# Kernel tuning notes

Hardware: AMD Instinct MI355X
Metric: run time of the kernel (lower is better)

The kernel has to match this reference:

```python
import jax, jax.numpy as jnp
import numpy as np

B, S, D = 8, 2048, 768
N_SPANS = 512
MAX_W = 30  # static max span width (inclusive width in tokens)
H = 100
NEG = -1e30


def setup_inputs() -> dict:
    key = jax.random.key(0)
    k1, k2, k3, k4, k5, k6 = jax.random.split(key, 6)
    seq_tensor = jax.random.normal(k1, (B, S, D), dtype=jnp.float32)
    starts = jax.random.randint(k2, (B, N_SPANS), 0, S - MAX_W)
    widths = jax.random.randint(k3, (B, N_SPANS), 1, MAX_W + 1)  # span length in [1, MAX_W]
    ends_excl = starts + widths  # exclusive end, as module expects
    span_indices = jnp.stack([starts, ends_excl], axis=-1).astype(jnp.int64)
    span_mask = (jax.random.uniform(k4, (B, N_SPANS)) > 0.1).astype(jnp.int32)
    att_w = jax.random.normal(k5, (D, 1), dtype=jnp.float32) / np.sqrt(D)
    att_b = jnp.zeros((1,), dtype=jnp.float32)
    ffnn_w = jax.random.normal(k6, (D, H), dtype=jnp.float32) / np.sqrt(D)
    ffnn_b = jnp.zeros((H,), dtype=jnp.float32)
    return {"seq_tensor": seq_tensor, "span_indices": span_indices, "span_mask": span_mask,
            "att_w": att_w, "att_b": att_b, "ffnn_w": ffnn_w, "ffnn_b": ffnn_b}


def reference(seq_tensor, span_indices, span_mask, att_w, att_b, ffnn_w, ffnn_b):
    # exclusive end -> inclusive end (span_end_is_exclusive=True)
    starts = span_indices[..., 0]
    ends = span_indices[..., 1] - 1
    widths = ends - starts  # inclusive width - 1, in [0, MAX_W-1]

    offsets = jnp.arange(MAX_W)  # [W]
    raw_idx = starts[..., None] + offsets  # [B, N, W]
    width_mask = offsets <= widths[..., None]  # [B, N, W]
    idx = jnp.where(width_mask, raw_idx, 0)

    # global attention logits over the sequence: [B, S]
    att_logits = (jnp.einsum('bsd,do->bso', seq_tensor, att_w) + att_b)[..., 0]

    # gather span token embeddings and logits: [B, N, W, D], [B, N, W]
    span_emb = jax.vmap(lambda seq, i: seq[i])(seq_tensor, idx)
    span_logits = jax.vmap(lambda lg, i: lg[i])(att_logits, idx)

    # masked softmax over span width
    span_logits = jnp.where(width_mask, span_logits, NEG)
    attn = jax.nn.softmax(span_logits, axis=-1)  # [B, N, W]

    attended = jnp.einsum('bnw,bnwd->bnd', attn, span_emb)  # [B, N, D]
    attended = attended * span_mask.astype(attended.dtype)[..., None]

    # FeedForward: 1 layer Linear + tanh (dropout=0)
    out = jnp.tanh(jnp.einsum('bnd,dh->bnh', attended, ffnn_w) + ffnn_b)
    return out
```

## Files before the change

kernel.cpp:

```cpp
#include <hip/hip_runtime.h>
#include <cstdint>
#include <cstddef>

#define NB 8
#define NS 2048
#define ND 768
#define NSP 512
#define MAXW 30
#define NH 100
#define LDP 104
#define NKS 24
#define NCF 8
#define BM 16
#define NIT 12

typedef __attribute__((ext_vector_type(8))) _Float16 half8;
typedef __attribute__((ext_vector_type(2))) __fp16 fp16x2;
typedef __attribute__((ext_vector_type(4))) float floatx4;

union U4H8 { uint4 v; half8 h8; unsigned u[4]; unsigned short us[8]; };
union H2U  { fp16x2 h; unsigned u; };

__device__ inline unsigned short f2h(float f) {
    _Float16 h = (_Float16)f;
    union { _Float16 hh; unsigned short us; } c; c.hh = h;
    return c.us;
}

__global__ __launch_bounds__(64) void pack_b_kernel(
    const float* __restrict__ ffnn_w, const float* __restrict__ att_w,
    uint4* __restrict__ Bfrag)
{
    const int ks = blockIdx.x >> 3, cf = blockIdx.x & 7;
    const int lane = threadIdx.x;
    const int q = lane >> 4, r = lane & 15;
    const int n = cf * 16 + r;
    U4H8 p;
#pragma unroll
    for (int j = 0; j < 8; j++) {
        int k = ks * 32 + q * 8 + j;
        float v = (n < NH) ? ffnn_w[(size_t)k * NH + n]
                           : (n == NH ? att_w[k] : 0.f);
        p.us[j] = f2h(v);
    }
    Bfrag[(size_t)(ks * NCF + cf) * 64 + lane] = p.v;
}

__global__ __launch_bounds__(256, 4) void proj_kernel(
    const float* __restrict__ seq, const uint4* __restrict__ Bfrag,
    float* __restrict__ P, float* __restrict__ Lg)
{
    __shared__ unsigned Ah[2][BM][36];
    const int t = threadIdx.x;
    const int wave = t >> 6, lane = t & 63;
    const int q = lane >> 4, r = lane & 15;
    const int cf0 = wave * 2;
    const int row0 = blockIdx.x * BM;

    floatx4 acc[2] = {{0.f,0.f,0.f,0.f},{0.f,0.f,0.f,0.f}};

    const int sr = t >> 4, sc = t & 15;
    const floatx4* gA = (const floatx4*)(seq + (size_t)(row0 + sr) * ND);
    floatx4 sv = __builtin_nontemporal_load(gA + sc);

    const uint4* bp = Bfrag + (size_t)cf0 * 64 + lane;
    uint4 Bc0 = bp[0], Bc1 = bp[64], Bc2 = bp[512], Bc3 = bp[512 + 64];

    for (int i = 0; i < NIT; ++i) {
        H2U u01, u23;
        u01.h = __builtin_amdgcn_cvt_pkrtz(sv.x, sv.y);
        u23.h = __builtin_amdgcn_cvt_pkrtz(sv.z, sv.w);
        { uint2 u; u.x = u01.u; u.y = u23.u; *(uint2*)&Ah[i & 1][sr][sc * 2] = u; }
        __syncthreads();

        const int ni = (i + 1 < NIT) ? i + 1 : i;
        sv = __builtin_nontemporal_load(gA + ni * 16 + sc);
        const size_t nb = (size_t)ni * 1024;
        uint4 Bn0 = bp[nb], Bn1 = bp[nb + 64], Bn2 = bp[nb + 512], Bn3 = bp[nb + 512 + 64];

#pragma unroll
        for (int ksl = 0; ksl < 2; ++ksl) {
            U4H8 a, b0, b1;
            a.v  = *(const uint4*)&Ah[i & 1][r][ksl * 16 + q * 4];
            b0.v = ksl ? Bc2 : Bc0;
            b1.v = ksl ? Bc3 : Bc1;
            acc[0] = __builtin_amdgcn_mfma_f32_16x16x32_f16(a.h8, b0.h8, acc[0], 0, 0, 0);
            acc[1] = __builtin_amdgcn_mfma_f32_16x16x32_f16(a.h8, b1.h8, acc[1], 0, 0, 0);
        }
        Bc0 = Bn0; Bc1 = Bn1; Bc2 = Bn2; Bc3 = Bn3;
    }

#pragma unroll
    for (int c = 0; c < 2; ++c) {
        const int col = (cf0 + c) * 16 + r;
        const int rowb = row0 + q * 4;
        if (col < NH) {
#pragma unroll
            for (int reg = 0; reg < 4; ++reg)
                P[(size_t)(rowb + reg) * LDP + col] = acc[c][reg];
        } else if (col == NH) {
#pragma unroll
            for (int reg = 0; reg < 4; ++reg)
                Lg[rowb + reg] = acc[c][reg];
        }
    }
}

__global__ __launch_bounds__(256, 4) void span_kernel(
    const int* __restrict__ span_idx, const int* __restrict__ span_mask,
    const float* __restrict__ P, const float* __restrict__ Lg,
    const float* __restrict__ ffnn_b, float* __restrict__ out)
{
    const int hw = threadIdx.x >> 5, lane = threadIdx.x & 31;
    const int gs = blockIdx.x * 8 + hw;
    const int b = gs / NSP;
    const int st = span_idx[2 * gs];
    int w = span_idx[2 * gs + 1] - st;
    w = max(1, min(w, MAXW));

    float lg = (lane < w) ? Lg[b * NS + st + lane] : -1e30f;
    float mx = lg;
#pragma unroll
    for (int off = 16; off > 0; off >>= 1) mx = fmaxf(mx, __shfl_xor(mx, off, 32));
    float e = (lane < w) ? __expf(lg - mx) : 0.f;
    float sum = e;
#pragma unroll
    for (int off = 16; off > 0; off >>= 1) sum += __shfl_xor(sum, off, 32);
    float attn = e / sum;

    int cl = min(lane, 24);
    const float4* Pb4 = (const float4*)(P + ((size_t)b * NS + st) * LDP) + cl;
    float4 acc = {0.f, 0.f, 0.f, 0.f};
#pragma unroll
    for (int i = 0; i < MAXW; ++i) {
        float a = __shfl(attn, i, 32);
        if (i < w) {
            float4 v = Pb4[i * (LDP / 4)];
            acc.x += a * v.x; acc.y += a * v.y; acc.z += a * v.z; acc.w += a * v.w;
        }
    }

    if (lane < 25) {
        float m = (float)span_mask[gs];
        float4 bias = ((const float4*)ffnn_b)[lane];
        float4 o;
        o.x = tanhf(m * acc.x + bias.x);
        o.y = tanhf(m * acc.y + bias.y);
        o.z = tanhf(m * acc.z + bias.z);
        o.w = tanhf(m * acc.w + bias.w);
        *(float4*)(out + (size_t)gs * NH + 4 * lane) = o;
    }
}

extern "C" void kernel_launch(void* const* d_in, const int* in_sizes, int n_in,
                              void* d_out, int out_size, void* d_ws, size_t ws_size,
                              hipStream_t stream) {
    const float* seq      = (const float*)d_in[0];
    const int*   span_idx = (const int*)d_in[1];
    const int*   span_msk = (const int*)d_in[2];
    const float* att_w    = (const float*)d_in[3];
    const float* ffnn_w   = (const float*)d_in[5];
    const float* ffnn_b   = (const float*)d_in[6];
    float* out = (float*)d_out;

    char* ws = (char*)d_ws;
    size_t off = 0;
    float* P     = (float*)(ws + off); off += (size_t)NB * NS * LDP * 4;
    uint4* Bfrag = (uint4*)(ws + off); off += (size_t)NKS * NCF * 64 * 16;
    float* Lg    = (float*)(ws + off);

    pack_b_kernel<<<NKS * NCF, 64, 0, stream>>>(ffnn_w, att_w, Bfrag);
    proj_kernel<<<(NB * NS) / BM, 256, 0, stream>>>(seq, Bfrag, P, Lg);
    span_kernel<<<(NB * NSP) / 8, 256, 0, stream>>>(span_idx, span_msk, P, Lg, ffnn_b, out);
}
```

Measured before the change: 122.4 us.

## Double projection row tile to 32 rows per block to reuse B fragments

Each proj_kernel block now covers 32 sequence rows instead of 16. Every wave reuses its loaded weight fragments across two 16-row MFMA tiles, which halves B-fragment global traffic per row and halves the block count. The A-tile staging changes so each thread loads two float4 per k-step, and the nontemporal loads become regular loads. The cost is more registers and accumulators per thread, which may lower occupancy, and fewer blocks to hide latency in what is likely a bandwidth-bound read of the sequence.

New measurement: 113.8 us. -7.0%, faster.

```diff
diff --git a/kernel.cpp b/kernel.cpp
--- a/kernel.cpp
+++ b/kernel.cpp
@@ -11,7 +11,7 @@
 #define LDP 104
 #define NKS 24
 #define NCF 8
-#define BM 16
+#define BM 32
 #define NIT 12
 
 typedef __attribute__((ext_vector_type(8))) _Float16 half8;
@@ -57,51 +57,63 @@
     const int cf0 = wave * 2;
     const int row0 = blockIdx.x * BM;
 
-    floatx4 acc[2] = {{0.f,0.f,0.f,0.f},{0.f,0.f,0.f,0.f}};
+    floatx4 acc[2][2] = {{{0.f,0.f,0.f,0.f},{0.f,0.f,0.f,0.f}},
+                         {{0.f,0.f,0.f,0.f},{0.f,0.f,0.f,0.f}}};
 
-    const int sr = t >> 4, sc = t & 15;
-    const floatx4* gA = (const floatx4*)(seq + (size_t)(row0 + sr) * ND);
-    floatx4 sv = __builtin_nontemporal_load(gA + sc);
+    const int sr = t >> 3, sc = t & 7;
+    const float4* gA = (const float4*)(seq + (size_t)(row0 + sr) * ND);
+    float4 sv0 = gA[sc], sv1 = gA[sc + 8];
 
     const uint4* bp = Bfrag + (size_t)cf0 * 64 + lane;
     uint4 Bc0 = bp[0], Bc1 = bp[64], Bc2 = bp[512], Bc3 = bp[512 + 64];
 
     for (int i = 0; i < NIT; ++i) {
-        H2U u01, u23;
-        u01.h = __builtin_amdgcn_cvt_pkrtz(sv.x, sv.y);
-        u23.h = __builtin_amdgcn_cvt_pkrtz(sv.z, sv.w);
-        { uint2 u; u.x = u01.u; u.y = u23.u; *(uint2*)&Ah[i & 1][sr][sc * 2] = u; }
+        H2U a01, a23, b01, b23;
+        a01.h = __builtin_amdgcn_cvt_pkrtz(sv0.x, sv0.y);
+        a23.h = __builtin_amdgcn_cvt_pkrtz(sv0.z, sv0.w);
+        b01.h = __builtin_amdgcn_cvt_pkrtz(sv1.x, sv1.y);
+        b23.h = __builtin_amdgcn_cvt_pkrtz(sv1.z, sv1.w);
+        { uint2 u; u.x = a01.u; u.y = a23.u; *(uint2*)&Ah[i & 1][sr][sc * 2] = u; }
+        { uint2 u; u.x = b01.u; u.y = b23.u; *(uint2*)&Ah[i & 1][sr][sc * 2 + 16] = u; }
         __syncthreads();
 
         const int ni = (i + 1 < NIT) ? i + 1 : i;
-        sv = __builtin_nontemporal_load(gA + ni * 16 + sc);
+        sv0 = gA[ni * 16 + sc];
+        sv1 = gA[ni * 16 + sc + 8];
         const size_t nb = (size_t)ni * 1024;
         uint4 Bn0 = bp[nb], Bn1 = bp[nb + 64], Bn2 = bp[nb + 512], Bn3 = bp[nb + 512 + 64];
 
 #pragma unroll
         for (int ksl = 0; ksl < 2; ++ksl) {
-            U4H8 a, b0, b1;
-            a.v  = *(const uint4*)&Ah[i & 1][r][ksl * 16 + q * 4];
+            U4H8 b0, b1;
             b0.v = ksl ? Bc2 : Bc0;
             b1.v = ksl ? Bc3 : Bc1;
-            acc[0] = __builtin_amdgcn_mfma_f32_16x16x32_f16(a.h8, b0.h8, acc[0], 0, 0, 0);
-            acc[1] = __builtin_amdgcn_mfma_f32_16x16x32_f16(a.h8, b1.h8, acc[1], 0, 0, 0);
+#pragma unroll
+            for (int rt = 0; rt < 2; ++rt) {
+                U4H8 a;
+                a.v = *(const uint4*)&Ah[i & 1][rt * 16 + r][ksl * 16 + q * 4];
+                acc[rt][0] = __builtin_amdgcn_mfma_f32_16x16x32_f16(a.h8, b0.h8, acc[rt][0], 0, 0, 0);
+                acc[rt][1] = __builtin_amdgcn_mfma_f32_16x16x32_f16(a.h8, b1.h8, acc[rt][1], 0, 0, 0);
+            }
         }
         Bc0 = Bn0; Bc1 = Bn1; Bc2 = Bn2; Bc3 = Bn3;
     }
 
 #pragma unroll
-    for (int c = 0; c < 2; ++c) {
-        const int col = (cf0 + c) * 16 + r;
-        const int rowb = row0 + q * 4;
-        if (col < NH) {
+    for (int rt = 0; rt < 2; ++rt) {
 #pragma unroll
-            for (int reg = 0; reg < 4; ++reg)
-                P[(size_t)(rowb + reg) * LDP + col] = acc[c][reg];
-        } else if (col == NH) {
+        for (int c = 0; c < 2; ++c) {
+            const int col = (cf0 + c) * 16 + r;
+            const int rowb = row0 + rt * 16 + q * 4;
+            if (col < NH) {
 #pragma unroll
-            for (int reg = 0; reg < 4; ++reg)
-                Lg[rowb + reg] = acc[c][reg];
+                for (int reg = 0; reg < 4; ++reg)
+                    P[(size_t)(rowb + reg) * LDP + col] = acc[rt][c][reg];
+            } else if (col == NH) {
+#pragma unroll
+                for (int reg = 0; reg < 4; ++reg)
+                    Lg[rowb + reg] = acc[rt][c][reg];
+            }
         }
     }
 }
```
